# Optimization experiments

Hardware: AMD Instinct MI355X
Metric: run time of the kernel (lower is better)

The kernel has to match this reference:

```python
import jax, jax.numpy as jnp
import numpy as np

N_NODES = 50000
N_EDGES = 800000
NUM_GRAPHS = 256
EPS = 1e-5


def _gcn_conv(x, edge_index, W, b):
    # PyG GCNConv: add self-loops, sym-normalize, aggregate, then add bias.
    n = x.shape[0]
    xw = x @ W  # [N, out]
    loops = jnp.arange(n)
    row = jnp.concatenate([edge_index[0], loops])  # source
    col = jnp.concatenate([edge_index[1], loops])  # target
    deg = jax.ops.segment_sum(jnp.ones_like(col, dtype=xw.dtype), col, num_segments=n)
    dinv = jnp.where(deg > 0, jax.lax.rsqrt(deg), 0.0)
    norm = dinv[row] * dinv[col]  # [E+N]
    msg = norm[:, None] * xw[row]  # gather + scale
    out = jax.ops.segment_sum(msg, col, num_segments=n)  # scatter-add
    return out + b


def _bn(x, g, b, m, v):
    # inference-mode batch norm
    return (x - m) * jax.lax.rsqrt(v + EPS) * g + b


def reference(x, edge_index, batch, gcn_W0, gcn_b0, bn_g0, bn_b0, bn_m0, bn_v0,
              gcn_W1, gcn_b1, bn_g1, bn_b1, bn_m1, bn_v1,
              hW1, hb1, hg1, hbb1, hm1, hv1,
              hW2, hb2, hg2, hbb2, hm2, hv2,
              hW3, hb3, hW4, hb4):
    # GCN block 0
    h = _gcn_conv(x, edge_index, gcn_W0, gcn_b0)
    h = jax.nn.relu(_bn(h, bn_g0, bn_b0, bn_m0, bn_v0))  # dropout = identity (eval)
    # GCN block 1
    h = _gcn_conv(h, edge_index, gcn_W1, gcn_b1)
    h = jax.nn.relu(_bn(h, bn_g1, bn_b1, bn_m1, bn_v1))
    # global mean pool over graphs
    sums = jax.ops.segment_sum(h, batch, num_segments=NUM_GRAPHS)
    cnts = jax.ops.segment_sum(jnp.ones_like(batch, dtype=h.dtype), batch, num_segments=NUM_GRAPHS)
    pooled = sums / jnp.maximum(cnts, 1.0)[:, None]  # [G, 64]
    # MLP head (eval: dropout identity)
    z = jax.nn.relu(_bn(pooled @ hW1 + hb1, hg1, hbb1, hm1, hv1))
    z = jax.nn.relu(_bn(z @ hW2 + hb2, hg2, hbb2, hm2, hv2))
    z = jax.nn.relu(z @ hW3 + hb3)
    out = (z @ hW4 + hb4).reshape(-1)  # [G]
    return out


def setup_inputs() -> dict:
    key = jax.random.key(0)
    ks = jax.random.split(key, 12)
    d = 64
    inp = {
        'x': jax.random.normal(ks[0], (N_NODES, d), dtype=jnp.float32),
        'edge_index': jax.random.randint(ks[1], (2, N_EDGES), 0, N_NODES, dtype=jnp.int64),
        'batch': jnp.sort(jax.random.randint(ks[2], (N_NODES,), 0, NUM_GRAPHS, dtype=jnp.int64)),
        'gcn_W0': jax.random.normal(ks[3], (d, d), dtype=jnp.float32) * 0.1,
        'gcn_b0': jnp.zeros((d,), jnp.float32),
        'bn_g0': jnp.ones((d,), jnp.float32), 'bn_b0': jnp.zeros((d,), jnp.float32),
        'bn_m0': jnp.zeros((d,), jnp.float32), 'bn_v0': jnp.ones((d,), jnp.float32),
        'gcn_W1': jax.random.normal(ks[4], (d, d), dtype=jnp.float32) * 0.1,
        'gcn_b1': jnp.zeros((d,), jnp.float32),
        'bn_g1': jnp.ones((d,), jnp.float32), 'bn_b1': jnp.zeros((d,), jnp.float32),
        'bn_m1': jnp.zeros((d,), jnp.float32), 'bn_v1': jnp.ones((d,), jnp.float32),
        'hW1': jax.random.normal(ks[5], (d, 256), dtype=jnp.float32) * 0.1,
        'hb1': jnp.zeros((256,), jnp.float32),
        'hg1': jnp.ones((256,), jnp.float32), 'hbb1': jnp.zeros((256,), jnp.float32),
        'hm1': jnp.zeros((256,), jnp.float32), 'hv1': jnp.ones((256,), jnp.float32),
        'hW2': jax.random.normal(ks[6], (256, 128), dtype=jnp.float32) * 0.1,
        'hb2': jnp.zeros((128,), jnp.float32),
        'hg2': jnp.ones((128,), jnp.float32), 'hbb2': jnp.zeros((128,), jnp.float32),
        'hm2': jnp.zeros((128,), jnp.float32), 'hv2': jnp.ones((128,), jnp.float32),
        'hW3': jax.random.normal(ks[7], (128, 64), dtype=jnp.float32) * 0.1,
        'hb3': jnp.zeros((64,), jnp.float32),
        'hW4': jax.random.normal(ks[8], (64, 1), dtype=jnp.float32) * 0.1,
        'hb4': jnp.zeros((1,), jnp.float32),
    }
    return inp
```

## Files before the change

kernel.cpp:

```cpp
#include <hip/hip_runtime.h>
#include <hip/hip_bf16.h>
#include <hip/hip_fp16.h>

#define N_NODES 50000
#define N_EDGES 800000
#define NUM_GRAPHS 256
#define D 64
#define EPS 1e-5f
#define N_PART 8
#define PART_SIZE (N_NODES / N_PART)
#define SCAT_CHUNKS 512
#define WP 72

typedef _Float16 half8_t __attribute__((ext_vector_type(8)));
typedef float f32x4 __attribute__((ext_vector_type(4)));

__global__ __launch_bounds__(256) void scatter_cnt_kernel(
        const int* __restrict__ ei, int* __restrict__ cnt,
        unsigned short* __restrict__ ssrc, int cap, int E) {
    int p     = blockIdx.x & (N_PART - 1);
    int chunk = blockIdx.x >> 3;
    int per   = (E + SCAT_CHUNKS - 1) / SCAT_CHUNKS;
    int lo    = chunk * per;
    int hi    = lo + per; if (hi > E) hi = E;
    for (int e = lo + threadIdx.x; e < hi; e += 256) {
        int c = ei[E + e];
        if (c / PART_SIZE == p) {
            int r = ei[e];
            int pos = atomicAdd(&cnt[c], 1);
            if (pos < cap) ssrc[(size_t)c * cap + pos] = (unsigned short)r;
        }
    }
}

__global__ __launch_bounds__(256) void gemm64_kernel(const float* __restrict__ X,
                                                     const float* __restrict__ W,
                                                     const int* __restrict__ cnt,
                                                     __half* __restrict__ Yh, int N) {
    __shared__ _Float16 Xs[64 * WP];
    __shared__ _Float16 Wt[64 * WP];
    int tid  = threadIdx.x;
    int base = blockIdx.x * 64;
    for (int i = tid; i < 4096; i += 256) {
        int k = i >> 6, n = i & 63;
        Wt[n * WP + k] = (_Float16)W[i];
    }
    for (int i = tid; i < 1024; i += 256) {
        int r = i >> 4, c4 = (i & 15) * 4;
        float4 xv = (base + r < N)
            ? ((const float4*)X)[(size_t)(base + r) * 16 + (i & 15)]
            : make_float4(0.f, 0.f, 0.f, 0.f);
        _Float16* dst = &Xs[r * WP + c4];
        dst[0] = (_Float16)xv.x; dst[1] = (_Float16)xv.y;
        dst[2] = (_Float16)xv.z; dst[3] = (_Float16)xv.w;
    }
    __syncthreads();
    int wave  = tid >> 6;
    int lane  = tid & 63;
    int m     = lane & 15;
    int q     = lane >> 4;
    int row16 = wave * 16;
    half8_t a0 = *(const half8_t*)&Xs[(row16 + m) * WP + q * 8];
    half8_t a1 = *(const half8_t*)&Xs[(row16 + m) * WP + 32 + q * 8];
    f32x4 acc[4];
#pragma unroll
    for (int ct = 0; ct < 4; ct++) {
        half8_t b0 = *(const half8_t*)&Wt[(ct * 16 + m) * WP + q * 8];
        half8_t b1 = *(const half8_t*)&Wt[(ct * 16 + m) * WP + 32 + q * 8];
        f32x4 c = {0.f, 0.f, 0.f, 0.f};
        c = __builtin_amdgcn_mfma_f32_16x16x32_f16(a0, b0, c, 0, 0, 0);
        c = __builtin_amdgcn_mfma_f32_16x16x32_f16(a1, b1, c, 0, 0, 0);
        acc[ct] = c;
    }
    int   rows[4];
    float ws[4];
#pragma unroll
    for (int reg = 0; reg < 4; reg++) {
        rows[reg] = base + row16 + q * 4 + reg;
        ws[reg] = (rows[reg] < N) ? rsqrtf((float)cnt[rows[reg]] + 1.0f) : 0.0f;
    }
#pragma unroll
    for (int ct = 0; ct < 4; ct++) {
#pragma unroll
        for (int reg = 0; reg < 4; reg++) {
            if (rows[reg] < N)
                Yh[(size_t)rows[reg] * 64 + ct * 16 + m] =
                    (__half)(ws[reg] * acc[ct][reg]);
        }
    }
}

__global__ __launch_bounds__(256) void agg_bn_kernel(
        const __half* __restrict__ xwh, const int* __restrict__ cnt,
        const unsigned short* __restrict__ ssrc, int cap,
        const float* __restrict__ b, const float* __restrict__ g,
        const float* __restrict__ bb, const float* __restrict__ m,
        const float* __restrict__ var,
        float* __restrict__ out, int N) {
    int wave = (blockIdx.x * blockDim.x + threadIdx.x) >> 6;
    int lane = threadIdx.x & 63;
    if (wave >= N) return;
    int c   = wave;
    int sub = lane >> 3;
    int f2  = lane & 7;
    const uint4* xw8 = (const uint4*)xwh;
    int n = cnt[c];
    if (n > cap) n = cap;
    size_t base = (size_t)c * cap;
    float dc = rsqrtf((float)n + 1.0f);
    float4 accA = make_float4(0.f, 0.f, 0.f, 0.f);
    float4 accB = accA;
    if (sub == 0) {
        uint4 v = xw8[(size_t)c * 8 + f2];
        __half2* hp = (__half2*)&v;
        float2 q0 = __half22float2(hp[0]), q1 = __half22float2(hp[1]);
        float2 q2 = __half22float2(hp[2]), q3 = __half22float2(hp[3]);
        accA.x = q0.x; accA.y = q0.y; accA.z = q1.x; accA.w = q1.y;
        accB.x = q2.x; accB.y = q2.y; accB.z = q3.x; accB.w = q3.y;
    }
    for (int e0 = 0; e0 < n; e0 += 8) {
        int e = e0 + sub;
        if (e < n) {
            int r = (int)ssrc[base + e];
            uint4 v = xw8[(size_t)r * 8 + f2];
            __half2* hp = (__half2*)&v;
            float2 q0 = __half22float2(hp[0]), q1 = __half22float2(hp[1]);
            float2 q2 = __half22float2(hp[2]), q3 = __half22float2(hp[3]);
            accA.x += q0.x; accA.y += q0.y;
            accA.z += q1.x; accA.w += q1.y;
            accB.x += q2.x; accB.y += q2.y;
            accB.z += q3.x; accB.w += q3.y;
        }
    }
#pragma unroll
    for (int off = 8; off < 64; off <<= 1) {
        accA.x += __shfl_xor(accA.x, off, 64); accA.y += __shfl_xor(accA.y, off, 64);
        accA.z += __shfl_xor(accA.z, off, 64); accA.w += __shfl_xor(accA.w, off, 64);
        accB.x += __shfl_xor(accB.x, off, 64); accB.y += __shfl_xor(accB.y, off, 64);
        accB.z += __shfl_xor(accB.z, off, 64); accB.w += __shfl_xor(accB.w, off, 64);
    }
    if (sub < 2) {
        int i4 = 2 * f2 + sub;
        float4 acc = sub ? accB : accA;
        float4 b4  = ((const float4*)b)[i4];
        float4 m4  = ((const float4*)m)[i4];
        float4 v4_ = ((const float4*)var)[i4];
        float4 g4  = ((const float4*)g)[i4];
        float4 bb4 = ((const float4*)bb)[i4];
        float4 h;
        h.x = (acc.x * dc + b4.x - m4.x) * (1.0f / sqrtf(v4_.x + EPS)) * g4.x + bb4.x;
        h.y = (acc.y * dc + b4.y - m4.y) * (1.0f / sqrtf(v4_.y + EPS)) * g4.y + bb4.y;
        h.z = (acc.z * dc + b4.z - m4.z) * (1.0f / sqrtf(v4_.z + EPS)) * g4.z + bb4.z;
        h.w = (acc.w * dc + b4.w - m4.w) * (1.0f / sqrtf(v4_.w + EPS)) * g4.w + bb4.w;
        h.x = h.x > 0.f ? h.x : 0.f;
        h.y = h.y > 0.f ? h.y : 0.f;
        h.z = h.z > 0.f ? h.z : 0.f;
        h.w = h.w > 0.f ? h.w : 0.f;
        ((float4*)out)[(size_t)c * 16 + i4] = h;
    }
}

__global__ __launch_bounds__(256) void pool_head_kernel(
        const float* __restrict__ h, const int* __restrict__ batch,
        const float* __restrict__ hW1, const float* __restrict__ hb1,
        const float* __restrict__ hg1, const float* __restrict__ hbb1,
        const float* __restrict__ hm1, const float* __restrict__ hv1,
        const float* __restrict__ hW2, const float* __restrict__ hb2,
        const float* __restrict__ hg2, const float* __restrict__ hbb2,
        const float* __restrict__ hm2, const float* __restrict__ hv2,
        const float* __restrict__ hW3, const float* __restrict__ hb3,
        const float* __restrict__ hW4, const float* __restrict__ hb4,
        float* __restrict__ out) {
    __shared__ int se[2];
    __shared__ float red[256];
    __shared__ float pooled[64];
    __shared__ float z1[256];
    __shared__ float z2[128];
    __shared__ float z3[64];
    int g = blockIdx.x;
    int t = threadIdx.x;
    if (t < 2) {
        int target = g + t;
        int lo = 0, hi = N_NODES;
        while (lo < hi) {
            int mid = (lo + hi) >> 1;
            if (batch[mid] < target) lo = mid + 1; else hi = mid;
        }
        se[t] = lo;
    }
    __syncthreads();
    int start = se[0], end = se[1];
    {
        int f = t & 63, rg = t >> 6;
        float part = 0.0f;
        for (int r = start + rg; r < end; r += 4) part += h[(size_t)r * 64 + f];
        red[t] = part;
        __syncthreads();
        if (t < 64) {
            float s = red[t] + red[t + 64] + red[t + 128] + red[t + 192];
            float cnt = (float)(end - start);
            cnt = cnt > 1.0f ? cnt : 1.0f;
            pooled[t] = s / cnt;
        }
    }
    __syncthreads();
    {
        float acc = hb1[t];
#pragma unroll
        for (int k = 0; k < 64; k++) acc += pooled[k] * hW1[k * 256 + t];
        acc = (acc - hm1[t]) * (1.0f / sqrtf(hv1[t] + EPS)) * hg1[t] + hbb1[t];
        z1[t] = acc > 0.0f ? acc : 0.0f;
    }
    __syncthreads();
    if (t < 128) {
        float acc = hb2[t];
#pragma unroll 8
        for (int k = 0; k < 256; k++) acc += z1[k] * hW2[k * 128 + t];
        acc = (acc - hm2[t]) * (1.0f / sqrtf(hv2[t] + EPS)) * hg2[t] + hbb2[t];
        z2[t] = acc > 0.0f ? acc : 0.0f;
    }
    __syncthreads();
    if (t < 64) {
        float acc = hb3[t];
#pragma unroll 8
        for (int k = 0; k < 128; k++) acc += z2[k] * hW3[k * 64 + t];
        z3[t] = acc > 0.0f ? acc : 0.0f;
    }
    __syncthreads();
    if (t < 64) {
        float v = z3[t] * hW4[t];
        for (int off = 32; off > 0; off >>= 1) v += __shfl_down(v, off, 64);
        if (t == 0) out[g] = v + hb4[0];
    }
}

extern "C" void kernel_launch(void* const* d_in, const int* in_sizes, int n_in,
                              void* d_out, int out_size, void* d_ws, size_t ws_size,
                              hipStream_t stream) {
    const float* x     = (const float*)d_in[0];
    const int*   ei    = (const int*)d_in[1];
    const int*   batch = (const int*)d_in[2];
    const float* W0 = (const float*)d_in[3];
    const float* b0 = (const float*)d_in[4];
    const float* g0 = (const float*)d_in[5];
    const float* bb0 = (const float*)d_in[6];
    const float* m0 = (const float*)d_in[7];
    const float* v0 = (const float*)d_in[8];
    const float* W1 = (const float*)d_in[9];
    const float* b1 = (const float*)d_in[10];
    const float* g1 = (const float*)d_in[11];
    const float* bb1 = (const float*)d_in[12];
    const float* m1 = (const float*)d_in[13];
    const float* v1 = (const float*)d_in[14];
    const float* hW1 = (const float*)d_in[15];
    const float* hb1 = (const float*)d_in[16];
    const float* hg1 = (const float*)d_in[17];
    const float* hbb1 = (const float*)d_in[18];
    const float* hm1 = (const float*)d_in[19];
    const float* hv1 = (const float*)d_in[20];
    const float* hW2 = (const float*)d_in[21];
    const float* hb2 = (const float*)d_in[22];
    const float* hg2 = (const float*)d_in[23];
    const float* hbb2 = (const float*)d_in[24];
    const float* hm2 = (const float*)d_in[25];
    const float* hv2 = (const float*)d_in[26];
    const float* hW3 = (const float*)d_in[27];
    const float* hb3 = (const float*)d_in[28];
    const float* hW4 = (const float*)d_in[29];
    const float* hb4 = (const float*)d_in[30];
    float* out = (float*)d_out;

    float*  bufA = (float*)d_ws;
    __half* xwh  = (__half*)bufA;
    float*  bufB = bufA + (size_t)N_NODES * D;
    int*    cnt  = (int*)(bufB + (size_t)N_NODES * D);
    unsigned short* ssrc = (unsigned short*)(cnt + N_NODES);

    size_t used  = ((size_t)2 * N_NODES * D + N_NODES) * 4;
    int cap = 64;
    if (ws_size >= used) {
        size_t avail = (ws_size - used) / ((size_t)N_NODES * 2);
        if (avail < (size_t)cap) cap = (int)avail & ~7;
    } else {
        cap = 0;
    }

    const int NT = 256;
    hipMemsetAsync(cnt, 0, (size_t)N_NODES * 4, stream);

    scatter_cnt_kernel<<<SCAT_CHUNKS * N_PART, NT, 0, stream>>>(ei, cnt, ssrc, cap, N_EDGES);

    gemm64_kernel<<<(N_NODES + 63) / 64, NT, 0, stream>>>(x, W0, cnt, xwh, N_NODES);
    agg_bn_kernel<<<(N_NODES * 64 + NT - 1) / NT, NT, 0, stream>>>(
        xwh, cnt, ssrc, cap, b0, g0, bb0, m0, v0, bufB, N_NODES);

    gemm64_kernel<<<(N_NODES + 63) / 64, NT, 0, stream>>>(bufB, W1, cnt, xwh, N_NODES);
    agg_bn_kernel<<<(N_NODES * 64 + NT - 1) / NT, NT, 0, stream>>>(
        xwh, cnt, ssrc, cap, b1, g1, bb1, m1, v1, bufB, N_NODES);

    pool_head_kernel<<<NUM_GRAPHS, NT, 0, stream>>>(bufB, batch,
        hW1, hb1, hg1, hbb1, hm1, hv1,
        hW2, hb2, hg2, hbb2, hm2, hv2,
        hW3, hb3, hW4, hb4, out);
}
```

Baseline: 267.1 us.

## Fuse graph build with GEMM0, aggregation with GEMM1, aggregation with pooling

Merges the edge-bucketing scatter and the first feature GEMM into one launch by giving them disjoint block ranges. The first aggregation with BN/ReLU is fused with the second GEMM through shared memory, and the second aggregation is fused with mean-pool accumulation via shared and global atomics. Source-degree normalization moves from the GEMM epilogue into the gather loop, adding an extra cnt load per edge. The intent is to remove the fp32 intermediate round trips and launch gaps. The cost is more atomics and lower parallelism per node, since each wave now walks 8 nodes in sequence.

Result: slower. 296.1 us (+10.9%).

```diff
diff --git a/kernel.cpp b/kernel.cpp
--- a/kernel.cpp
+++ b/kernel.cpp
@@ -10,44 +10,119 @@
 #define N_PART 8
 #define PART_SIZE (N_NODES / N_PART)
 #define SCAT_CHUNKS 512
+#define SCAT_GRID (SCAT_CHUNKS * N_PART)
+#define GEMM_BLOCKS ((N_NODES + 63) / 64)
 #define WP 72
 
 typedef _Float16 half8_t __attribute__((ext_vector_type(8)));
+typedef _Float16 half4_t __attribute__((ext_vector_type(4)));
 typedef float f32x4 __attribute__((ext_vector_type(4)));
 
-__global__ __launch_bounds__(256) void scatter_cnt_kernel(
+__device__ __forceinline__ void agg_node(const uint4* __restrict__ xw8,
+        const int* __restrict__ cnt, const unsigned short* __restrict__ ssrc,
+        int cap, int c, int sub, int f2,
+        float4& accA, float4& accB, float& dc) {
+    int n = cnt[c];
+    if (n > cap) n = cap;
+    dc = rsqrtf((float)n + 1.0f);
+    size_t sbase = (size_t)c * cap;
+    accA = make_float4(0.f, 0.f, 0.f, 0.f);
+    accB = accA;
+    if (sub == 0) {
+        uint4 v = xw8[(size_t)c * 8 + f2];
+        const __half2* hp = (const __half2*)&v;
+        float2 q0 = __half22float2(hp[0]), q1 = __half22float2(hp[1]);
+        float2 q2 = __half22float2(hp[2]), q3 = __half22float2(hp[3]);
+        accA.x = dc * q0.x; accA.y = dc * q0.y;
+        accA.z = dc * q1.x; accA.w = dc * q1.y;
+        accB.x = dc * q2.x; accB.y = dc * q2.y;
+        accB.z = dc * q3.x; accB.w = dc * q3.y;
+    }
+    for (int e0 = 0; e0 < n; e0 += 8) {
+        int e = e0 + sub;
+        if (e < n) {
+            int r = (int)ssrc[sbase + e];
+            float wr = rsqrtf((float)cnt[r] + 1.0f);
+            uint4 v = xw8[(size_t)r * 8 + f2];
+            const __half2* hp = (const __half2*)&v;
+            float2 q0 = __half22float2(hp[0]), q1 = __half22float2(hp[1]);
+            float2 q2 = __half22float2(hp[2]), q3 = __half22float2(hp[3]);
+            accA.x += wr * q0.x; accA.y += wr * q0.y;
+            accA.z += wr * q1.x; accA.w += wr * q1.y;
+            accB.x += wr * q2.x; accB.y += wr * q2.y;
+            accB.z += wr * q3.x; accB.w += wr * q3.y;
+        }
+    }
+#pragma unroll
+    for (int off = 8; off < 64; off <<= 1) {
+        accA.x += __shfl_xor(accA.x, off, 64); accA.y += __shfl_xor(accA.y, off, 64);
+        accA.z += __shfl_xor(accA.z, off, 64); accA.w += __shfl_xor(accA.w, off, 64);
+        accB.x += __shfl_xor(accB.x, off, 64); accB.y += __shfl_xor(accB.y, off, 64);
+        accB.z += __shfl_xor(accB.z, off, 64); accB.w += __shfl_xor(accB.w, off, 64);
+    }
+}
+
+__device__ __forceinline__ float4 bn_relu4(float4 acc, float dc, int i4,
+        const float* __restrict__ b, const float* __restrict__ g,
+        const float* __restrict__ bb, const float* __restrict__ m,
+        const float* __restrict__ var) {
+    float4 b4  = ((const float4*)b)[i4];
+    float4 m4  = ((const float4*)m)[i4];
+    float4 v4_ = ((const float4*)var)[i4];
+    float4 g4  = ((const float4*)g)[i4];
+    float4 bb4 = ((const float4*)bb)[i4];
+    float4 h;
+    h.x = (acc.x * dc + b4.x - m4.x) * (1.0f / sqrtf(v4_.x + EPS)) * g4.x + bb4.x;
+    h.y = (acc.y * dc + b4.y - m4.y) * (1.0f / sqrtf(v4_.y + EPS)) * g4.y + bb4.y;
+    h.z = (acc.z * dc + b4.z - m4.z) * (1.0f / sqrtf(v4_.z + EPS)) * g4.z + bb4.z;
+    h.w = (acc.w * dc + b4.w - m4.w) * (1.0f / sqrtf(v4_.w + EPS)) * g4.w + bb4.w;
+    h.x = h.x > 0.f ? h.x : 0.f;
+    h.y = h.y > 0.f ? h.y : 0.f;
+    h.z = h.z > 0.f ? h.z : 0.f;
+    h.w = h.w > 0.f ? h.w : 0.f;
+    return h;
+}
+
+__global__ __launch_bounds__(256) void build_gemm_kernel(
         const int* __restrict__ ei, int* __restrict__ cnt,
-        unsigned short* __restrict__ ssrc, int cap, int E) {
-    int p     = blockIdx.x & (N_PART - 1);
-    int chunk = blockIdx.x >> 3;
-    int per   = (E + SCAT_CHUNKS - 1) / SCAT_CHUNKS;
-    int lo    = chunk * per;
-    int hi    = lo + per; if (hi > E) hi = E;
-    for (int e = lo + threadIdx.x; e < hi; e += 256) {
-        int c = ei[E + e];
-        if (c / PART_SIZE == p) {
-            int r = ei[e];
-            int pos = atomicAdd(&cnt[c], 1);
-            if (pos < cap) ssrc[(size_t)c * cap + pos] = (unsigned short)r;
-        }
-    }
-}
-
-__global__ __launch_bounds__(256) void gemm64_kernel(const float* __restrict__ X,
-                                                     const float* __restrict__ W,
-                                                     const int* __restrict__ cnt,
-                                                     __half* __restrict__ Yh, int N) {
+        unsigned short* __restrict__ ssrc, int cap,
+        const float* __restrict__ X, const float* __restrict__ W,
+        __half* __restrict__ Yh) {
     __shared__ _Float16 Xs[64 * WP];
     __shared__ _Float16 Wt[64 * WP];
+    if (blockIdx.x < SCAT_GRID) {
+        int p     = blockIdx.x & (N_PART - 1);
+        int chunk = blockIdx.x >> 3;
+        const int per = (((N_EDGES + SCAT_CHUNKS - 1) / SCAT_CHUNKS) + 3) & ~3;
+        int lo = chunk * per;
+        int hi = lo + per; if (hi > N_EDGES) hi = N_EDGES;
+        for (int e4 = lo + (int)threadIdx.x * 4; e4 < hi; e4 += 1024) {
+            int4 c4 = *(const int4*)&ei[N_EDGES + e4];
+            const int* cc = (const int*)&c4;
+#pragma unroll
+            for (int k = 0; k < 4; k++) {
+                int e = e4 + k;
+                if (e < hi) {
+                    int c = cc[k];
+                    if (c / PART_SIZE == p) {
+                        int r = ei[e];
+                        int pos = atomicAdd(&cnt[c], 1);
+                        if (pos < cap) ssrc[(size_t)c * cap + pos] = (unsigned short)r;
+                    }
+                }
+            }
+        }
+        return;
+    }
     int tid  = threadIdx.x;
-    int base = blockIdx.x * 64;
+    int base = (blockIdx.x - SCAT_GRID) * 64;
     for (int i = tid; i < 4096; i += 256) {
         int k = i >> 6, n = i & 63;
         Wt[n * WP + k] = (_Float16)W[i];
     }
     for (int i = tid; i < 1024; i += 256) {
         int r = i >> 4, c4 = (i & 15) * 4;
-        float4 xv = (base + r < N)
+        float4 xv = (base + r < N_NODES)
             ? ((const float4*)X)[(size_t)(base + r) * 16 + (i & 15)]
             : make_float4(0.f, 0.f, 0.f, 0.f);
         _Float16* dst = &Xs[r * WP + c4];
@@ -72,96 +147,129 @@
         c = __builtin_amdgcn_mfma_f32_16x16x32_f16(a1, b1, c, 0, 0, 0);
         acc[ct] = c;
     }
-    int   rows[4];
-    float ws[4];
-#pragma unroll
-    for (int reg = 0; reg < 4; reg++) {
-        rows[reg] = base + row16 + q * 4 + reg;
-        ws[reg] = (rows[reg] < N) ? rsqrtf((float)cnt[rows[reg]] + 1.0f) : 0.0f;
-    }
 #pragma unroll
     for (int ct = 0; ct < 4; ct++) {
 #pragma unroll
         for (int reg = 0; reg < 4; reg++) {
-            if (rows[reg] < N)
-                Yh[(size_t)rows[reg] * 64 + ct * 16 + m] =
-                    (__half)(ws[reg] * acc[ct][reg]);
-        }
-    }
-}
-
-__global__ __launch_bounds__(256) void agg_bn_kernel(
-        const __half* __restrict__ xwh, const int* __restrict__ cnt,
+            int row = base + row16 + q * 4 + reg;
+            if (row < N_NODES)
+                Yh[(size_t)row * 64 + ct * 16 + m] = (__half)acc[ct][reg];
+        }
+    }
+}
+
+__global__ __launch_bounds__(512) void agg_gemm_kernel(
+        const __half* __restrict__ xwh_in, const int* __restrict__ cnt,
         const unsigned short* __restrict__ ssrc, int cap,
         const float* __restrict__ b, const float* __restrict__ g,
         const float* __restrict__ bb, const float* __restrict__ m,
         const float* __restrict__ var,
-        float* __restrict__ out, int N) {
-    int wave = (blockIdx.x * blockDim.x + threadIdx.x) >> 6;
-    int lane = threadIdx.x & 63;
-    if (wave >= N) return;
-    int c   = wave;
-    int sub = lane >> 3;
-    int f2  = lane & 7;
-    const uint4* xw8 = (const uint4*)xwh;
-    int n = cnt[c];
-    if (n > cap) n = cap;
-    size_t base = (size_t)c * cap;
-    float dc = rsqrtf((float)n + 1.0f);
-    float4 accA = make_float4(0.f, 0.f, 0.f, 0.f);
-    float4 accB = accA;
-    if (sub == 0) {
-        uint4 v = xw8[(size_t)c * 8 + f2];
-        __half2* hp = (__half2*)&v;
-        float2 q0 = __half22float2(hp[0]), q1 = __half22float2(hp[1]);
-        float2 q2 = __half22float2(hp[2]), q3 = __half22float2(hp[3]);
-        accA.x = q0.x; accA.y = q0.y; accA.z = q1.x; accA.w = q1.y;
-        accB.x = q2.x; accB.y = q2.y; accB.z = q3.x; accB.w = q3.y;
-    }
-    for (int e0 = 0; e0 < n; e0 += 8) {
-        int e = e0 + sub;
-        if (e < n) {
-            int r = (int)ssrc[base + e];
-            uint4 v = xw8[(size_t)r * 8 + f2];
-            __half2* hp = (__half2*)&v;
-            float2 q0 = __half22float2(hp[0]), q1 = __half22float2(hp[1]);
-            float2 q2 = __half22float2(hp[2]), q3 = __half22float2(hp[3]);
-            accA.x += q0.x; accA.y += q0.y;
-            accA.z += q1.x; accA.w += q1.y;
-            accB.x += q2.x; accB.y += q2.y;
-            accB.z += q3.x; accB.w += q3.y;
-        }
-    }
-#pragma unroll
-    for (int off = 8; off < 64; off <<= 1) {
-        accA.x += __shfl_xor(accA.x, off, 64); accA.y += __shfl_xor(accA.y, off, 64);
-        accA.z += __shfl_xor(accA.z, off, 64); accA.w += __shfl_xor(accA.w, off, 64);
-        accB.x += __shfl_xor(accB.x, off, 64); accB.y += __shfl_xor(accB.y, off, 64);
-        accB.z += __shfl_xor(accB.z, off, 64); accB.w += __shfl_xor(accB.w, off, 64);
-    }
-    if (sub < 2) {
-        int i4 = 2 * f2 + sub;
-        float4 acc = sub ? accB : accA;
-        float4 b4  = ((const float4*)b)[i4];
-        float4 m4  = ((const float4*)m)[i4];
-        float4 v4_ = ((const float4*)var)[i4];
-        float4 g4  = ((const float4*)g)[i4];
-        float4 bb4 = ((const float4*)bb)[i4];
-        float4 h;
-        h.x = (acc.x * dc + b4.x - m4.x) * (1.0f / sqrtf(v4_.x + EPS)) * g4.x + bb4.x;
-        h.y = (acc.y * dc + b4.y - m4.y) * (1.0f / sqrtf(v4_.y + EPS)) * g4.y + bb4.y;
-        h.z = (acc.z * dc + b4.z - m4.z) * (1.0f / sqrtf(v4_.z + EPS)) * g4.z + bb4.z;
-        h.w = (acc.w * dc + b4.w - m4.w) * (1.0f / sqrtf(v4_.w + EPS)) * g4.w + bb4.w;
-        h.x = h.x > 0.f ? h.x : 0.f;
-        h.y = h.y > 0.f ? h.y : 0.f;
-        h.z = h.z > 0.f ? h.z : 0.f;
-        h.w = h.w > 0.f ? h.w : 0.f;
-        ((float4*)out)[(size_t)c * 16 + i4] = h;
-    }
-}
-
-__global__ __launch_bounds__(256) void pool_head_kernel(
-        const float* __restrict__ h, const int* __restrict__ batch,
+        const float* __restrict__ W, __half* __restrict__ xwh_out, int N) {
+    __shared__ _Float16 Xs[64 * WP];
+    __shared__ _Float16 Wt[64 * WP];
+    int tid = threadIdx.x;
+    for (int i = tid; i < 4096; i += 512) {
+        int k = i >> 6, n = i & 63;
+        Wt[n * WP + k] = (_Float16)W[i];
+    }
+    int wave = tid >> 6, lane = tid & 63;
+    int sub = lane >> 3, f2 = lane & 7;
+    int base = blockIdx.x * 64;
+    const uint4* xw8 = (const uint4*)xwh_in;
+    for (int i = 0; i < 8; i++) {
+        int idx = wave * 8 + i;
+        int c = base + idx;
+        if (c < N) {
+            float4 accA, accB; float dc;
+            agg_node(xw8, cnt, ssrc, cap, c, sub, f2, accA, accB, dc);
+            if (sub < 2) {
+                int i4 = 2 * f2 + sub;
+                float4 h = bn_relu4(sub ? accB : accA, dc, i4, b, g, bb, m, var);
+                half4_t hv = {(_Float16)h.x, (_Float16)h.y, (_Float16)h.z, (_Float16)h.w};
+                *(half4_t*)&Xs[idx * WP + i4 * 4] = hv;
+            }
+        } else if (sub < 2) {
+            int i4 = 2 * f2 + sub;
+            half4_t hv = {(_Float16)0.f, (_Float16)0.f, (_Float16)0.f, (_Float16)0.f};
+            *(half4_t*)&Xs[idx * WP + i4 * 4] = hv;
+        }
+    }
+    __syncthreads();
+    int m_ = lane & 15, q = lane >> 4;
+#pragma unroll
+    for (int tt = 0; tt < 2; tt++) {
+        int t   = wave + tt * 8;
+        int r16 = (t >> 2) * 16;
+        int ct  = t & 3;
+        half8_t a0 = *(const half8_t*)&Xs[(r16 + m_) * WP + q * 8];
+        half8_t a1 = *(const half8_t*)&Xs[(r16 + m_) * WP + 32 + q * 8];
+        half8_t b0 = *(const half8_t*)&Wt[(ct * 16 + m_) * WP + q * 8];
+        half8_t b1 = *(const half8_t*)&Wt[(ct * 16 + m_) * WP + 32 + q * 8];
+        f32x4 cc = {0.f, 0.f, 0.f, 0.f};
+        cc = __builtin_amdgcn_mfma_f32_16x16x32_f16(a0, b0, cc, 0, 0, 0);
+        cc = __builtin_amdgcn_mfma_f32_16x16x32_f16(a1, b1, cc, 0, 0, 0);
+#pragma unroll
+        for (int reg = 0; reg < 4; reg++) {
+            int row = base + r16 + q * 4 + reg;
+            if (row < N)
+                xwh_out[(size_t)row * 64 + ct * 16 + m_] = (__half)cc[reg];
+        }
+    }
+}
+
+__global__ __launch_bounds__(512) void agg_pool_kernel(
+        const __half* __restrict__ xwh_in, const int* __restrict__ cnt,
+        const unsigned short* __restrict__ ssrc, int cap,
+        const float* __restrict__ b, const float* __restrict__ g,
+        const float* __restrict__ bb, const float* __restrict__ m,
+        const float* __restrict__ var,
+        const int* __restrict__ batch, float* __restrict__ sums, int N) {
+    __shared__ float gsum[4][64];
+    __shared__ int ginfo[2];
+    int tid = threadIdx.x;
+    if (tid < 256) gsum[tid >> 6][tid & 63] = 0.0f;
+    int base = blockIdx.x * 64;
+    if (tid == 0) {
+        int last = base + 63; if (last >= N) last = N - 1;
+        int glo = batch[base];
+        ginfo[0] = glo;
+        ginfo[1] = batch[last] - glo + 1;
+    }
+    __syncthreads();
+    int glo = ginfo[0], span = ginfo[1];
+    int wave = tid >> 6, lane = tid & 63;
+    int sub = lane >> 3, f2 = lane & 7;
+    const uint4* xw8 = (const uint4*)xwh_in;
+    for (int i = 0; i < 8; i++) {
+        int idx = wave * 8 + i;
+        int c = base + idx;
+        if (c >= N) continue;
+        float4 accA, accB; float dc;
+        agg_node(xw8, cnt, ssrc, cap, c, sub, f2, accA, accB, dc);
+        if (sub < 2) {
+            int i4 = 2 * f2 + sub;
+            float4 h = bn_relu4(sub ? accB : accA, dc, i4, b, g, bb, m, var);
+            int gid = batch[c];
+            if (span <= 4) {
+                float* gp = &gsum[gid - glo][i4 * 4];
+                atomicAdd(&gp[0], h.x); atomicAdd(&gp[1], h.y);
+                atomicAdd(&gp[2], h.z); atomicAdd(&gp[3], h.w);
+            } else {
+                float* sp = &sums[(size_t)gid * 64 + i4 * 4];
+                atomicAdd(&sp[0], h.x); atomicAdd(&sp[1], h.y);
+                atomicAdd(&sp[2], h.z); atomicAdd(&sp[3], h.w);
+            }
+        }
+    }
+    __syncthreads();
+    if (span <= 4 && tid < span * 64) {
+        float v = gsum[tid >> 6][tid & 63];
+        atomicAdd(&sums[(size_t)(glo + (tid >> 6)) * 64 + (tid & 63)], v);
+    }
+}
+
+__global__ __launch_bounds__(256) void head_kernel(
+        const float* __restrict__ sums, const int* __restrict__ batch,
         const float* __restrict__ hW1, const float* __restrict__ hb1,
         const float* __restrict__ hg1, const float* __restrict__ hbb1,
         const float* __restrict__ hm1, const float* __restrict__ hv1,
@@ -172,7 +280,6 @@
         const float* __restrict__ hW4, const float* __restrict__ hb4,
         float* __restrict__ out) {
     __shared__ int se[2];
-    __shared__ float red[256];
     __shared__ float pooled[64];
     __shared__ float z1[256];
     __shared__ float z2[128];
@@ -189,19 +296,10 @@
         se[t] = lo;
     }
     __syncthreads();
-    int start = se[0], end = se[1];
-    {
-        int f = t & 63, rg = t >> 6;
-        float part = 0.0f;
-        for (int r = start + rg; r < end; r += 4) part += h[(size_t)r * 64 + f];
-        red[t] = part;
-        __syncthreads();
-        if (t < 64) {
-            float s = red[t] + red[t + 64] + red[t + 128] + red[t + 192];
-            float cnt = (float)(end - start);
-            cnt = cnt > 1.0f ? cnt : 1.0f;
-            pooled[t] = s / cnt;
-        }
+    if (t < 64) {
+        float cntf = (float)(se[1] - se[0]);
+        cntf = cntf > 1.0f ? cntf : 1.0f;
+        pooled[t] = sums[(size_t)g * 64 + t] / cntf;
     }
     __syncthreads();
     {
@@ -270,13 +368,14 @@
     const float* hb4 = (const float*)d_in[30];
     float* out = (float*)d_out;
 
-    float*  bufA = (float*)d_ws;
-    __half* xwh  = (__half*)bufA;
-    float*  bufB = bufA + (size_t)N_NODES * D;
-    int*    cnt  = (int*)(bufB + (size_t)N_NODES * D);
-    unsigned short* ssrc = (unsigned short*)(cnt + N_NODES);
-
-    size_t used  = ((size_t)2 * N_NODES * D + N_NODES) * 4;
+    __half* xwhA = (__half*)d_ws;
+    __half* xwhB = xwhA + (size_t)N_NODES * D;
+    int*    cnt  = (int*)(xwhB + (size_t)N_NODES * D);
+    float*  sums = (float*)(cnt + N_NODES);
+    unsigned short* ssrc = (unsigned short*)(sums + NUM_GRAPHS * D);
+
+    size_t used = (size_t)2 * N_NODES * D * 2 + (size_t)N_NODES * 4
+                + (size_t)NUM_GRAPHS * D * 4;
     int cap = 64;
     if (ws_size >= used) {
         size_t avail = (ws_size - used) / ((size_t)N_NODES * 2);
@@ -285,20 +384,18 @@
         cap = 0;
     }
 
-    const int NT = 256;
-    hipMemsetAsync(cnt, 0, (size_t)N_NODES * 4, stream);
-
-    scatter_cnt_kernel<<<SCAT_CHUNKS * N_PART, NT, 0, stream>>>(ei, cnt, ssrc, cap, N_EDGES);
-
-    gemm64_kernel<<<(N_NODES + 63) / 64, NT, 0, stream>>>(x, W0, cnt, xwh, N_NODES);
-    agg_bn_kernel<<<(N_NODES * 64 + NT - 1) / NT, NT, 0, stream>>>(
-        xwh, cnt, ssrc, cap, b0, g0, bb0, m0, v0, bufB, N_NODES);
-
-    gemm64_kernel<<<(N_NODES + 63) / 64, NT, 0, stream>>>(bufB, W1, cnt, xwh, N_NODES);
-    agg_bn_kernel<<<(N_NODES * 64 + NT - 1) / NT, NT, 0, stream>>>(
-        xwh, cnt, ssrc, cap, b1, g1, bb1, m1, v1, bufB, N_NODES);
-
-    pool_head_kernel<<<NUM_GRAPHS, NT, 0, stream>>>(bufB, batch,
+    hipMemsetAsync(cnt, 0, (size_t)N_NODES * 4 + (size_t)NUM_GRAPHS * D * 4, stream);
+
+    build_gemm_kernel<<<SCAT_GRID + GEMM_BLOCKS, 256, 0, stream>>>(
+        ei, cnt, ssrc, cap, x, W0, xwhA);
+
+    agg_gemm_kernel<<<GEMM_BLOCKS, 512, 0, stream>>>(
+        xwhA, cnt, ssrc, cap, b0, g0, bb0, m0, v0, W1, xwhB, N_NODES);
+
+    agg_pool_kernel<<<GEMM_BLOCKS, 512, 0, stream>>>(
+        xwhB, cnt, ssrc, cap, b1, g1, bb1, m1, v1, batch, sums, N_NODES);
+
+    head_kernel<<<NUM_GRAPHS, 256, 0, stream>>>(sums, batch,
         hW1, hb1, hg1, hbb1, hm1, hv1,
         hW2, hb2, hg2, hbb2, hm2, hv2,
         hW3, hb3, hW4, hb4, out);
```

## Fuse edge bucketing with first GEMM and software-pipeline aggregation gathers

Applied to the files above, without the earlier changes.

Merges the edge scatter/count kernel and the first XW GEMM into one launch, so the independent GEMM blocks can overlap the atomic-heavy bucketing. The degree scaling for layer 0 moves into a separate small scale kernel. The aggregation kernel now loads up to 64 neighbour indices with one coalesced load, passes them around with shuffles, and prefetches the next neighbour row before accumulating the current one. The costs are an extra launch and an extra pass over the layer-0 features for scaling, plus a second half-precision buffer in the workspace.

Measured after the change: 261.7 us. 2.0% less time.

```diff
diff --git a/kernel.cpp b/kernel.cpp
--- a/kernel.cpp
+++ b/kernel.cpp
@@ -10,44 +10,61 @@
 #define N_PART 8
 #define PART_SIZE (N_NODES / N_PART)
 #define SCAT_CHUNKS 512
+#define SCAT_GRID (SCAT_CHUNKS * N_PART)
+#define GEMM_BLOCKS ((N_NODES + 63) / 64)
 #define WP 72
 
 typedef _Float16 half8_t __attribute__((ext_vector_type(8)));
 typedef float f32x4 __attribute__((ext_vector_type(4)));
 
-__global__ __launch_bounds__(256) void scatter_cnt_kernel(
+__device__ __forceinline__ void acc16(const uint4& v, float w, float4& A, float4& B) {
+    const __half2* hp = (const __half2*)&v;
+    float2 q0 = __half22float2(hp[0]), q1 = __half22float2(hp[1]);
+    float2 q2 = __half22float2(hp[2]), q3 = __half22float2(hp[3]);
+    A.x += w * q0.x; A.y += w * q0.y; A.z += w * q1.x; A.w += w * q1.y;
+    B.x += w * q2.x; B.y += w * q2.y; B.z += w * q3.x; B.w += w * q3.y;
+}
+
+__global__ __launch_bounds__(256) void build_gemm_kernel(
         const int* __restrict__ ei, int* __restrict__ cnt,
-        unsigned short* __restrict__ ssrc, int cap, int E) {
-    int p     = blockIdx.x & (N_PART - 1);
-    int chunk = blockIdx.x >> 3;
-    int per   = (E + SCAT_CHUNKS - 1) / SCAT_CHUNKS;
-    int lo    = chunk * per;
-    int hi    = lo + per; if (hi > E) hi = E;
-    for (int e = lo + threadIdx.x; e < hi; e += 256) {
-        int c = ei[E + e];
-        if (c / PART_SIZE == p) {
-            int r = ei[e];
-            int pos = atomicAdd(&cnt[c], 1);
-            if (pos < cap) ssrc[(size_t)c * cap + pos] = (unsigned short)r;
-        }
-    }
-}
-
-__global__ __launch_bounds__(256) void gemm64_kernel(const float* __restrict__ X,
-                                                     const float* __restrict__ W,
-                                                     const int* __restrict__ cnt,
-                                                     __half* __restrict__ Yh, int N) {
+        unsigned short* __restrict__ ssrc, int cap,
+        const float* __restrict__ X, const float* __restrict__ W,
+        __half* __restrict__ Yh) {
     __shared__ _Float16 Xs[64 * WP];
     __shared__ _Float16 Wt[64 * WP];
+    if (blockIdx.x < SCAT_GRID) {
+        int p     = blockIdx.x & (N_PART - 1);
+        int chunk = blockIdx.x >> 3;
+        const int per = (((N_EDGES + SCAT_CHUNKS - 1) / SCAT_CHUNKS) + 3) & ~3;
+        int lo = chunk * per;
+        int hi = lo + per; if (hi > N_EDGES) hi = N_EDGES;
+        for (int e4 = lo + (int)threadIdx.x * 4; e4 < hi; e4 += 1024) {
+            int4 c4 = *(const int4*)&ei[N_EDGES + e4];
+            const int* cc = (const int*)&c4;
+#pragma unroll
+            for (int k = 0; k < 4; k++) {
+                int e = e4 + k;
+                if (e < hi) {
+                    int c = cc[k];
+                    if (c / PART_SIZE == p) {
+                        int r = ei[e];
+                        int pos = atomicAdd(&cnt[c], 1);
+                        if (pos < cap) ssrc[(size_t)c * cap + pos] = (unsigned short)r;
+                    }
+                }
+            }
+        }
+        return;
+    }
     int tid  = threadIdx.x;
-    int base = blockIdx.x * 64;
+    int base = (blockIdx.x - SCAT_GRID) * 64;
     for (int i = tid; i < 4096; i += 256) {
         int k = i >> 6, n = i & 63;
         Wt[n * WP + k] = (_Float16)W[i];
     }
     for (int i = tid; i < 1024; i += 256) {
         int r = i >> 4, c4 = (i & 15) * 4;
-        float4 xv = (base + r < N)
+        float4 xv = (base + r < N_NODES)
             ? ((const float4*)X)[(size_t)(base + r) * 16 + (i & 15)]
             : make_float4(0.f, 0.f, 0.f, 0.f);
         _Float16* dst = &Xs[r * WP + c4];
@@ -72,22 +89,32 @@
         c = __builtin_amdgcn_mfma_f32_16x16x32_f16(a1, b1, c, 0, 0, 0);
         acc[ct] = c;
     }
-    int   rows[4];
-    float ws[4];
-#pragma unroll
-    for (int reg = 0; reg < 4; reg++) {
-        rows[reg] = base + row16 + q * 4 + reg;
-        ws[reg] = (rows[reg] < N) ? rsqrtf((float)cnt[rows[reg]] + 1.0f) : 0.0f;
-    }
 #pragma unroll
     for (int ct = 0; ct < 4; ct++) {
 #pragma unroll
         for (int reg = 0; reg < 4; reg++) {
-            if (rows[reg] < N)
-                Yh[(size_t)rows[reg] * 64 + ct * 16 + m] =
-                    (__half)(ws[reg] * acc[ct][reg]);
-        }
-    }
+            int row = base + row16 + q * 4 + reg;
+            if (row < N_NODES)
+                Yh[(size_t)row * 64 + ct * 16 + m] = (__half)acc[ct][reg];
+        }
+    }
+}
+
+__global__ __launch_bounds__(256) void scale_kernel(__half* __restrict__ xwh,
+                                                    const int* __restrict__ cnt,
+                                                    int N) {
+    int i = blockIdx.x * 256 + threadIdx.x;
+    if (i >= N * 8) return;
+    int row = i >> 3;
+    float w = rsqrtf((float)cnt[row] + 1.0f);
+    uint4 v = ((const uint4*)xwh)[i];
+    __half2* hp = (__half2*)&v;
+#pragma unroll
+    for (int j = 0; j < 4; j++) {
+        float2 q = __half22float2(hp[j]);
+        hp[j] = __floats2half2_rn(q.x * w, q.y * w);
+    }
+    ((uint4*)xwh)[i] = v;
 }
 
 __global__ __launch_bounds__(256) void agg_bn_kernel(
@@ -106,32 +133,33 @@
     const uint4* xw8 = (const uint4*)xwh;
     int n = cnt[c];
     if (n > cap) n = cap;
-    size_t base = (size_t)c * cap;
     float dc = rsqrtf((float)n + 1.0f);
+    size_t sbase = (size_t)c * cap;
+    int idx = (lane < cap) ? (int)ssrc[sbase + lane] : 0;
+    uint4 vself = make_uint4(0u, 0u, 0u, 0u);
+    if (sub == 0) vself = xw8[(size_t)c * 8 + f2];
+    int t = (n + 7) >> 3;
     float4 accA = make_float4(0.f, 0.f, 0.f, 0.f);
     float4 accB = accA;
-    if (sub == 0) {
-        uint4 v = xw8[(size_t)c * 8 + f2];
-        __half2* hp = (__half2*)&v;
-        float2 q0 = __half22float2(hp[0]), q1 = __half22float2(hp[1]);
-        float2 q2 = __half22float2(hp[2]), q3 = __half22float2(hp[3]);
-        accA.x = q0.x; accA.y = q0.y; accA.z = q1.x; accA.w = q1.y;
-        accB.x = q2.x; accB.y = q2.y; accB.z = q3.x; accB.w = q3.y;
-    }
-    for (int e0 = 0; e0 < n; e0 += 8) {
-        int e = e0 + sub;
-        if (e < n) {
-            int r = (int)ssrc[base + e];
-            uint4 v = xw8[(size_t)r * 8 + f2];
-            __half2* hp = (__half2*)&v;
-            float2 q0 = __half22float2(hp[0]), q1 = __half22float2(hp[1]);
-            float2 q2 = __half22float2(hp[2]), q3 = __half22float2(hp[3]);
-            accA.x += q0.x; accA.y += q0.y;
-            accA.z += q1.x; accA.w += q1.y;
-            accB.x += q2.x; accB.y += q2.y;
-            accB.z += q3.x; accB.w += q3.y;
-        }
-    }
+    uint4 vc = make_uint4(0u, 0u, 0u, 0u);
+    float wc = 0.0f;
+    if (t > 0) {
+        int r0 = __shfl(idx, sub, 64);
+        wc = (sub < n) ? 1.0f : 0.0f;
+        if (sub >= n) r0 = c;
+        vc = xw8[(size_t)r0 * 8 + f2];
+    }
+    for (int k = 1; k < t; k++) {
+        int s  = k * 8 + sub;
+        int r1 = __shfl(idx, s, 64);
+        float wn = (s < n) ? 1.0f : 0.0f;
+        if (s >= n) r1 = c;
+        uint4 vn = xw8[(size_t)r1 * 8 + f2];
+        acc16(vc, wc, accA, accB);
+        vc = vn; wc = wn;
+    }
+    if (t > 0) acc16(vc, wc, accA, accB);
+    if (sub == 0) acc16(vself, 1.0f, accA, accB);
 #pragma unroll
     for (int off = 8; off < 64; off <<= 1) {
         accA.x += __shfl_xor(accA.x, off, 64); accA.y += __shfl_xor(accA.y, off, 64);
@@ -157,6 +185,63 @@
         h.z = h.z > 0.f ? h.z : 0.f;
         h.w = h.w > 0.f ? h.w : 0.f;
         ((float4*)out)[(size_t)c * 16 + i4] = h;
+    }
+}
+
+__global__ __launch_bounds__(256) void gemm64_kernel(const float* __restrict__ X,
+                                                     const float* __restrict__ W,
+                                                     const int* __restrict__ cnt,
+                                                     __half* __restrict__ Yh, int N) {
+    __shared__ _Float16 Xs[64 * WP];
+    __shared__ _Float16 Wt[64 * WP];
+    int tid  = threadIdx.x;
+    int base = blockIdx.x * 64;
+    for (int i = tid; i < 4096; i += 256) {
+        int k = i >> 6, n = i & 63;
+        Wt[n * WP + k] = (_Float16)W[i];
+    }
+    for (int i = tid; i < 1024; i += 256) {
+        int r = i >> 4, c4 = (i & 15) * 4;
+        float4 xv = (base + r < N)
+            ? ((const float4*)X)[(size_t)(base + r) * 16 + (i & 15)]
+            : make_float4(0.f, 0.f, 0.f, 0.f);
+        _Float16* dst = &Xs[r * WP + c4];
+        dst[0] = (_Float16)xv.x; dst[1] = (_Float16)xv.y;
+        dst[2] = (_Float16)xv.z; dst[3] = (_Float16)xv.w;
+    }
+    __syncthreads();
+    int wave  = tid >> 6;
+    int lane  = tid & 63;
+    int m     = lane & 15;
+    int q     = lane >> 4;
+    int row16 = wave * 16;
+    half8_t a0 = *(const half8_t*)&Xs[(row16 + m) * WP + q * 8];
+    half8_t a1 = *(const half8_t*)&Xs[(row16 + m) * WP + 32 + q * 8];
+    f32x4 acc[4];
+#pragma unroll
+    for (int ct = 0; ct < 4; ct++) {
+        half8_t b0 = *(const half8_t*)&Wt[(ct * 16 + m) * WP + q * 8];
+        half8_t b1 = *(const half8_t*)&Wt[(ct * 16 + m) * WP + 32 + q * 8];
+        f32x4 c = {0.f, 0.f, 0.f, 0.f};
+        c = __builtin_amdgcn_mfma_f32_16x16x32_f16(a0, b0, c, 0, 0, 0);
+        c = __builtin_amdgcn_mfma_f32_16x16x32_f16(a1, b1, c, 0, 0, 0);
+        acc[ct] = c;
+    }
+    int   rows[4];
+    float ws[4];
+#pragma unroll
+    for (int reg = 0; reg < 4; reg++) {
+        rows[reg] = base + row16 + q * 4 + reg;
+        ws[reg] = (rows[reg] < N) ? rsqrtf((float)cnt[rows[reg]] + 1.0f) : 0.0f;
+    }
+#pragma unroll
+    for (int ct = 0; ct < 4; ct++) {
+#pragma unroll
+        for (int reg = 0; reg < 4; reg++) {
+            if (rows[reg] < N)
+                Yh[(size_t)rows[reg] * 64 + ct * 16 + m] =
+                    (__half)(ws[reg] * acc[ct][reg]);
+        }
     }
 }
 
@@ -270,13 +355,14 @@
     const float* hb4 = (const float*)d_in[30];
     float* out = (float*)d_out;
 
-    float*  bufA = (float*)d_ws;
-    __half* xwh  = (__half*)bufA;
-    float*  bufB = bufA + (size_t)N_NODES * D;
+    __half* xwhA = (__half*)d_ws;
+    __half* xwhB = xwhA + (size_t)N_NODES * D;
+    float*  bufB = (float*)(xwhB + (size_t)N_NODES * D);
     int*    cnt  = (int*)(bufB + (size_t)N_NODES * D);
     unsigned short* ssrc = (unsigned short*)(cnt + N_NODES);
 
-    size_t used  = ((size_t)2 * N_NODES * D + N_NODES) * 4;
+    size_t used = (size_t)2 * N_NODES * D * 2 + (size_t)N_NODES * D * 4
+                + (size_t)N_NODES * 4;
     int cap = 64;
     if (ws_size >= used) {
         size_t avail = (ws_size - used) / ((size_t)N_NODES * 2);
@@ -288,15 +374,18 @@
     const int NT = 256;
     hipMemsetAsync(cnt, 0, (size_t)N_NODES * 4, stream);
 
-    scatter_cnt_kernel<<<SCAT_CHUNKS * N_PART, NT, 0, stream>>>(ei, cnt, ssrc, cap, N_EDGES);
-
-    gemm64_kernel<<<(N_NODES + 63) / 64, NT, 0, stream>>>(x, W0, cnt, xwh, N_NODES);
-    agg_bn_kernel<<<(N_NODES * 64 + NT - 1) / NT, NT, 0, stream>>>(
-        xwh, cnt, ssrc, cap, b0, g0, bb0, m0, v0, bufB, N_NODES);
-
-    gemm64_kernel<<<(N_NODES + 63) / 64, NT, 0, stream>>>(bufB, W1, cnt, xwh, N_NODES);
-    agg_bn_kernel<<<(N_NODES * 64 + NT - 1) / NT, NT, 0, stream>>>(
-        xwh, cnt, ssrc, cap, b1, g1, bb1, m1, v1, bufB, N_NODES);
+    build_gemm_kernel<<<SCAT_GRID + GEMM_BLOCKS, NT, 0, stream>>>(
+        ei, cnt, ssrc, cap, x, W0, xwhA);
+
+    scale_kernel<<<(N_NODES * 8 + NT - 1) / NT, NT, 0, stream>>>(xwhA, cnt, N_NODES);
+
+    agg_bn_kernel<<<(N_NODES * 64) / NT, NT, 0, stream>>>(
+        xwhA, cnt, ssrc, cap, b0, g0, bb0, m0, v0, bufB, N_NODES);
+
+    gemm64_kernel<<<GEMM_BLOCKS, NT, 0, stream>>>(bufB, W1, cnt, xwhB, N_NODES);
+
+    agg_bn_kernel<<<(N_NODES * 64) / NT, NT, 0, stream>>>(
+        xwhB, cnt, ssrc, cap, b1, g1, bb1, m1, v1, bufB, N_NODES);
 
     pool_head_kernel<<<NUM_GRAPHS, NT, 0, stream>>>(bufB, batch,
         hW1, hb1, hg1, hbb1, hm1, hv1,
```
